# Performance work log

Hardware: AMD Instinct MI355X
Metric: run time of the kernel (lower is better)

Reference implementation:

```python
import jax, jax.numpy as jnp
import numpy as np

D_MODEL = 1024
NUM_HEADS = 16
D_HEAD = D_MODEL // NUM_HEADS


def setup_inputs() -> dict:
    key = jax.random.key(0)
    ks = jax.random.split(key, 5)
    b, n = 4, 2048
    x = jax.random.normal(ks[0], (b, n, D_MODEL), dtype=jnp.float32)
    s = 1.0 / np.sqrt(D_MODEL)
    w_qkv = jax.random.normal(ks[1], (D_MODEL, 3 * D_MODEL), dtype=jnp.float32) * s
    b_qkv = jax.random.normal(ks[2], (3 * D_MODEL,), dtype=jnp.float32) * 0.01
    w_out = jax.random.normal(ks[3], (D_MODEL, D_MODEL), dtype=jnp.float32) * s
    b_out = jax.random.normal(ks[4], (D_MODEL,), dtype=jnp.float32) * 0.01
    return {"x": x, "w_qkv": w_qkv, "b_qkv": b_qkv, "w_out": w_out, "b_out": b_out}


def reference(x, w_qkv, b_qkv, w_out, b_out):
    b, n, _ = x.shape
    h, d = NUM_HEADS, D_HEAD
    scale = d ** -0.5
    qkv = x @ w_qkv + b_qkv                       # [b, n, 3*d_model]
    # split as (qkv, h, d) on the feature axis, matching 'b n (qkv h d)'
    qkv = qkv.reshape(b, n, 3, h, d).transpose(2, 0, 3, 1, 4)  # [3, b, h, n, d]
    q, k, v = qkv[0], qkv[1], qkv[2]
    dots = jnp.einsum('bhid,bhjd->bhij', q, k) * scale
    causal = jnp.tril(jnp.ones((n, n), dtype=bool))
    dots = jnp.where(causal[None, None], dots, -jnp.inf)
    attn = jax.nn.softmax(dots, axis=-1)
    out = jnp.einsum('bhij,bhjd->bhid', attn, v)
    out = out.transpose(0, 2, 1, 3).reshape(b, n, h * d)
    return out @ w_out + b_out
```

## Files before the change

kernel.cpp:

```cpp
#include <hip/hip_runtime.h>
#include <hip/hip_bf16.h>
#include <stdint.h>

typedef unsigned short u16;
typedef __attribute__((ext_vector_type(8))) short bf16x8;
typedef __attribute__((ext_vector_type(4))) float f32x4;
typedef __attribute__((ext_vector_type(16))) float f32x16;
typedef __attribute__((ext_vector_type(4))) short s16x4;
typedef __attribute__((ext_vector_type(2))) unsigned u32x2;

#define SEQ   2048
#define BATCH 4

#define MFMA16(a,b,c) __builtin_amdgcn_mfma_f32_16x16x32_bf16(a,b,c,0,0,0)
#define MFMA32(a,b,c) __builtin_amdgcn_mfma_f32_32x32x16_bf16(a,b,c,0,0,0)
#define EXP2F __builtin_amdgcn_exp2f

__device__ __forceinline__ u16 f2bf(float f) {
  union { float f; uint32_t u; } c{f};
  uint32_t r = c.u + 0x7fffu + ((c.u >> 16) & 1u);
  return (u16)(r >> 16);
}

__device__ __forceinline__ void gll16(const void* g, void* l) {
  __builtin_amdgcn_global_load_lds((const __attribute__((address_space(1))) void*)g,
                                   (__attribute__((address_space(3))) void*)l,
                                   16, 0, 0);
}

__device__ __forceinline__ void plswap(uint32_t &a, uint32_t &b) {
  u32x2 r = __builtin_amdgcn_permlane32_swap(a, b, false, false);
  a = r[0]; b = r[1];
}
__device__ __forceinline__ float xhalf_max(float v) {
  union { float f; uint32_t u; } c{v};
  u32x2 r = __builtin_amdgcn_permlane32_swap(c.u, c.u, false, false);
  union { uint32_t u; float f; } x{r[0]}, y{r[1]};
  return fmaxf(x.f, y.f);
}
__device__ __forceinline__ float xhalf_add(float v) {
  union { float f; uint32_t u; } c{v};
  u32x2 r = __builtin_amdgcn_permlane32_swap(c.u, c.u, false, false);
  union { uint32_t u; float f; } x{r[0]}, y{r[1]};
  return x.f + y.f;
}

__global__ __launch_bounds__(256) void k_prep(const float* __restrict__ x,
                                              u16* __restrict__ xbf,
                                              const float* __restrict__ wqkv,
                                              u16* __restrict__ wqkvT,
                                              const float* __restrict__ wout,
                                              u16* __restrict__ woutT) {
  __shared__ float tl[32][33];
  const int bid = blockIdx.x, t = threadIdx.x;
  if (bid < 4096) {
    int i = (bid * 256 + t) * 8;
    float4 a = *(const float4*)(x + i);
    float4 b = *(const float4*)(x + i + 4);
    union { u16 u[8]; bf16x8 v; } r;
    r.u[0] = f2bf(a.x); r.u[1] = f2bf(a.y); r.u[2] = f2bf(a.z); r.u[3] = f2bf(a.w);
    r.u[4] = f2bf(b.x); r.u[5] = f2bf(b.y); r.u[6] = f2bf(b.z); r.u[7] = f2bf(b.w);
    *(bf16x8*)(xbf + i) = r.v;
    return;
  }
  const float* in; u16* out; int N, idx, nx;
  if (bid < 4096 + 3072) { in = wqkv; out = wqkvT; N = 3072; idx = bid - 4096; nx = 96; }
  else                   { in = wout; out = woutT; N = 1024; idx = bid - 7168; nx = 32; }
  const int K = 1024;
  const int c0 = (idx % nx) * 32, r0 = (idx / nx) * 32;
  const int tx = t & 31, ty = t >> 5;
#pragma unroll
  for (int j = 0; j < 32; j += 8)
    tl[ty + j][tx] = in[(size_t)(r0 + ty + j) * N + c0 + tx];
  __syncthreads();
#pragma unroll
  for (int j = 0; j < 32; j += 8)
    out[(size_t)(c0 + ty + j) * K + r0 + tx] = f2bf(tl[tx][ty + j]);
}

#define SBAR  asm volatile("s_barrier" ::: "memory")
#define LGKM0 asm volatile("s_waitcnt lgkmcnt(0)" ::: "memory")
#define VM2   asm volatile("s_waitcnt vmcnt(2)" ::: "memory")
#define VM0   asm volatile("s_waitcnt vmcnt(0)" ::: "memory")
#define FEN   asm volatile("" ::: "memory")

template<int OUT_F32, int VSPLIT>
__global__ __launch_bounds__(512, 2) void k_gemm256(const u16* __restrict__ A,
                                                    const u16* __restrict__ BT,
                                                    const float* __restrict__ bias,
                                                    void* __restrict__ Cv,
                                                    u16* __restrict__ vT,
                                                    int N, int K, int NT, int TN) {
  __shared__ alignas(16) char LDS[81920];
  const int t = threadIdx.x;
  const int l = t & 63, w = t >> 6;
  const int wm = w >> 2, wn = w & 3;
  const int lr = l & 15, lg = l >> 4;

  const int nwg = gridDim.x;
  const int cpx = nwg >> 3;
  const int sb = (blockIdx.x & 7) * cpx + (blockIdx.x >> 3);
  const int brow = (sb / TN) * 256, bcol = (sb % TN) * 128;

  auto stageA = [&](int c, int h, int tt) {
#pragma unroll
    for (int i = 0; i < 2; i++) {
      int s = t + i * 512;
      int r = s >> 3, cg = s & 7;
      int grow = brow + (r >> 6) * 128 + h * 64 + (r & 63);
      int gk = tt * 64 + ((cg ^ (r & 7)) * 8);
      gll16(A + (size_t)grow * K + gk, LDS + c * 32768 + h * 16384 + s * 16);
    }
  };
  auto stageB = [&](int tt) {
#pragma unroll
    for (int i = 0; i < 2; i++) {
      int s = t + i * 512;
      int r = s >> 3, cg = s & 7;
      int grow = bcol + r;
      int gk = tt * 64 + ((cg ^ (r & 7)) * 8);
      gll16(BT + (size_t)grow * K + gk, LDS + 65536 + s * 16);
    }
  };

  f32x4 acc[8][2] = {};
  bf16x8 afr[4], bfr[2][2];

#define READ_A(c, h, ks)                                                       \
  {                                                                            \
    const char* baseA = LDS + (c) * 32768 + (h) * 16384 + (wm * 64) * 128;     \
    _Pragma("unroll") for (int mi = 0; mi < 4; mi++)                           \
      afr[mi] = *(const bf16x8*)(baseA + (mi * 16 + lr) * 128 +                \
                                 ((((ks) * 4 + lg) ^ (lr & 7)) * 16));         \
  }
#define READ_B_ALL()                                                           \
  {                                                                            \
    const char* baseB = LDS + 65536 + (wn * 32) * 128;                         \
    _Pragma("unroll") for (int ks = 0; ks < 2; ks++)                           \
      _Pragma("unroll") for (int ni = 0; ni < 2; ni++)                         \
        bfr[ks][ni] = *(const bf16x8*)(baseB + (ni * 16 + lr) * 128 +          \
                                       (((ks * 4 + lg) ^ (lr & 7)) * 16));     \
  }
#define DO_MFMA(H, KS)                                                         \
  {                                                                            \
    __builtin_amdgcn_s_setprio(1);                                             \
    _Pragma("unroll") for (int mi = 0; mi < 4; mi++)                           \
      _Pragma("unroll") for (int ni = 0; ni < 2; ni++)                         \
        acc[(H)*4 + mi][ni] = MFMA16(afr[mi], bfr[KS][ni], acc[(H)*4 + mi][ni]); \
    __builtin_amdgcn_s_setprio(0);                                             \
  }

  stageA(0, 0, 0); FEN;
  stageB(0);       FEN;
  stageA(0, 1, 0); FEN;
  VM2; SBAR;

  for (int tt = 0; tt < NT; tt++) {
    const int c = tt & 1;
    if (tt + 1 < NT) { stageA(c ^ 1, 0, tt + 1); FEN; }
    READ_A(c, 0, 0); READ_B_ALL();
    DO_MFMA(0, 0);
    if (tt + 1 < NT) { VM2; } else { VM0; }
    LGKM0; SBAR;
    if (tt + 1 < NT) { stageB(tt + 1); FEN; }
    READ_A(c, 1, 0);
    DO_MFMA(1, 0);
    if (tt + 1 < NT) { stageA(c ^ 1, 1, tt + 1); FEN; }
    READ_A(c, 1, 1);
    DO_MFMA(1, 1);
    READ_A(c, 0, 1);
    DO_MFMA(0, 1);
    if (tt + 1 < NT) { VM2; } else { VM0; }
    LGKM0; SBAR;
  }

  const int r0 = brow + wm * 128 + lg * 4;
  const int c0 = bcol + wn * 32 + lr;
#pragma unroll
  for (int ni = 0; ni < 2; ni++) {
    const int col = c0 + ni * 16;
    float bv = bias[col];
#pragma unroll
    for (int mig = 0; mig < 8; mig++) {
      const int row = r0 + mig * 16;
      if (VSPLIT && col >= 2048) {
        const int bb = row >> 11, n0 = row & 2047;
        union { u16 u[4]; s16x4 v; } pk4;
#pragma unroll
        for (int r = 0; r < 4; r++) pk4.u[r] = f2bf(acc[mig][ni][r] + bv);
        *(s16x4*)(vT + ((size_t)(bb * 1024 + col - 2048) * SEQ + n0)) = pk4.v;
      } else {
#pragma unroll
        for (int r = 0; r < 4; r++) {
          float v = acc[mig][ni][r] + bv;
          size_t off = (size_t)(row + r) * N + col;
          if (OUT_F32) ((float*)Cv)[off] = v;
          else         ((u16*)Cv)[off]   = f2bf(v);
        }
      }
    }
  }
}
#undef READ_A
#undef READ_B_ALL
#undef DO_MFMA

__global__ __launch_bounds__(256, 2) void k_attn(const u16* __restrict__ qkv,
                                                 const u16* __restrict__ vT,
                                                 u16* __restrict__ outp) {
  __shared__ alignas(16) char SB[2][16384];
  const int t = threadIdx.x, l = t & 63, w = t >> 6;
  const int hi = l >> 5, q = l & 31;
  const int h = blockIdx.x, qp = blockIdx.y, b = blockIdx.z;
  const int bh = b * 16 + h;
  const int srow = t >> 3;
  const int csw = ((t & 7) * 16) ^ ((srow & 7) << 4);
  const int swz = (q & 7) << 4;
  const float SC = 0.18033688011112042f;

  auto STAGE = [&](char* buf, int kv0) {
    char* lK = buf + w * 1024;
    char* lV = buf + 8192 + w * 1024;
    gll16(qkv + (size_t)(b * SEQ + kv0 + srow) * 3072 + 1024 + h * 64 + (csw >> 1), lK);
    gll16(qkv + (size_t)(b * SEQ + kv0 + srow + 32) * 3072 + 1024 + h * 64 + (csw >> 1), lK + 4096);
    gll16(vT + (size_t)(bh * 64 + srow) * SEQ + kv0 + (csw >> 1), lV);
    gll16(vT + (size_t)(bh * 64 + srow + 32) * SEQ + kv0 + (csw >> 1), lV + 4096);
  };

  auto COMPUTE = [&](const char* Kb, const char* Vb, int kv0, int qr0, int qg,
                     const bf16x8* qf, f32x16& o0, f32x16& o1, f32x16& lv,
                     float& m_run) {
    f32x16 st0 = {}, st1 = {};
    __builtin_amdgcn_s_setprio(1);
#pragma unroll
    for (int c = 0; c < 4; c++) {
      const int cb = c * 32 + hi * 16;
      bf16x8 k0 = *(const bf16x8*)(Kb + q * 128 + (cb ^ swz));
      bf16x8 k1 = *(const bf16x8*)(Kb + (32 + q) * 128 + (cb ^ swz));
      st0 = MFMA32(k0, qf[c], st0);
      st1 = MFMA32(k1, qf[c], st1);
    }
    __builtin_amdgcn_s_setprio(0);
    if (kv0 + 63 > qr0) {
#pragma unroll
      for (int r = 0; r < 16; r++) {
        const int krow = (r & 3) + 8 * (r >> 2) + 4 * hi;
        if (kv0 + krow > qg)      st0[r] = -1e30f;
        if (kv0 + 32 + krow > qg) st1[r] = -1e30f;
      }
    }
    float tmx[16];
#pragma unroll
    for (int r = 0; r < 16; r++) tmx[r] = fmaxf(st0[r], st1[r]);
    float v0 = fmaxf(fmaxf(tmx[0], tmx[1]), tmx[2]);
    float v1 = fmaxf(fmaxf(tmx[3], tmx[4]), tmx[5]);
    float v2 = fmaxf(fmaxf(tmx[6], tmx[7]), tmx[8]);
    float v3 = fmaxf(fmaxf(tmx[9], tmx[10]), tmx[11]);
    float v4 = fmaxf(fmaxf(tmx[12], tmx[13]), tmx[14]);
    float v5 = fmaxf(fmaxf(v0, v1), tmx[15]);
    float v6 = fmaxf(fmaxf(v2, v3), v4);
    float v7 = fmaxf(v5, v6);
    const float vs = xhalf_max(v7) * SC;
    if (__any(vs > m_run + 8.0f)) {
      float mnew = fmaxf(m_run, vs);
      float corr = EXP2F(m_run - mnew);
      m_run = mnew;
#pragma unroll
      for (int r = 0; r < 16; r++) { o0[r] *= corr; o1[r] *= corr; lv[r] *= corr; }
    }
    f32x16 e0 = st0 * SC - m_run;
    f32x16 e1 = st1 * SC - m_run;
    f32x16 p0, p1;
#pragma unroll
    for (int r = 0; r < 16; r++) { p0[r] = EXP2F(e0[r]); p1[r] = EXP2F(e1[r]); }
    lv += p0 + p1;
#pragma unroll
    for (int khb = 0; khb < 2; khb++) {
      uint32_t pk[8];
#pragma unroll
      for (int ii = 0; ii < 8; ii++) {
        float lo = khb ? p1[2 * ii] : p0[2 * ii];
        float hf = khb ? p1[2 * ii + 1] : p0[2 * ii + 1];
        asm("v_cvt_pk_bf16_f32 %0, %1, %2" : "=v"(pk[ii]) : "v"(lo), "v"(hf));
      }
      plswap(pk[0], pk[2]); plswap(pk[1], pk[3]);
      plswap(pk[4], pk[6]); plswap(pk[5], pk[7]);
      union { uint32_t u[4]; bf16x8 v; } be, bo;
      be.u[0] = pk[0]; be.u[1] = pk[1]; be.u[2] = pk[2]; be.u[3] = pk[3];
      bo.u[0] = pk[4]; bo.u[1] = pk[5]; bo.u[2] = pk[6]; bo.u[3] = pk[7];
      __builtin_amdgcn_s_setprio(1);
#pragma unroll
      for (int kti = 0; kti < 2; kti++) {
        const int cb = (khb * 2 + kti) * 32 + hi * 16;
        bf16x8 vv0 = *(const bf16x8*)(Vb + q * 128 + (cb ^ swz));
        bf16x8 vv1 = *(const bf16x8*)(Vb + (32 + q) * 128 + (cb ^ swz));
        bf16x8 pb = kti ? bo.v : be.v;
        o0 = MFMA32(vv0, pb, o0);
        o1 = MFMA32(vv1, pb, o1);
      }
      __builtin_amdgcn_s_setprio(0);
    }
  };

  const int qtA = qp, qtB = 15 - qp;
  const int qr0A = qtA * 128 + w * 32, qgA = qr0A + q;
  const int qr0B = qtB * 128 + w * 32, qgB = qr0B + q;
  bf16x8 qfA[4], qfB[4];
#pragma unroll
  for (int c = 0; c < 4; c++) {
    qfA[c] = *(const bf16x8*)(qkv + (size_t)(b * SEQ + qgA) * 3072 + h * 64 + c * 16 + hi * 8);
    qfB[c] = *(const bf16x8*)(qkv + (size_t)(b * SEQ + qgB) * 3072 + h * 64 + c * 16 + hi * 8);
  }
  f32x16 oA0 = {}, oA1 = {}, lvA = {};
  f32x16 oB0 = {}, oB1 = {}, lvB = {};
  float mA = -1e30f, mB = -1e30f;
  const int nkvB = 2 * qtB + 2;

  STAGE(SB[0], 0);
  for (int j = 0; j < nkvB; j++) {
    const int kv0 = j * 64;
    __syncthreads();
    if (j + 1 < nkvB) STAGE(SB[(j + 1) & 1], kv0 + 64);
    const char* Kb = SB[j & 1];
    const char* Vb = Kb + 8192;
    if (kv0 <= qr0A + 31)
      COMPUTE(Kb, Vb, kv0, qr0A, qgA, qfA, oA0, oA1, lvA, mA);
    if (kv0 <= qr0B + 31)
      COMPUTE(Kb, Vb, kv0, qr0B, qgB, qfB, oB0, oB1, lvB, mB);
  }
#pragma unroll
  for (int sel = 0; sel < 2; sel++) {
    f32x16& o0 = sel ? oB0 : oA0;
    f32x16& o1 = sel ? oB1 : oA1;
    f32x16& lv = sel ? lvB : lvA;
    const int qg = sel ? qgB : qgA;
    float ls = ((lv[0] + lv[1]) + (lv[2] + lv[3])) + ((lv[4] + lv[5]) + (lv[6] + lv[7]))
             + ((lv[8] + lv[9]) + (lv[10] + lv[11])) + ((lv[12] + lv[13]) + (lv[14] + lv[15]));
    ls = xhalf_add(ls);
    const float invl = 1.0f / ls;
#pragma unroll
    for (int dh = 0; dh < 2; dh++)
#pragma unroll
      for (int jq = 0; jq < 4; jq++) {
        union { u16 u[4]; s16x4 v; } pk4;
#pragma unroll
        for (int r = 0; r < 4; r++)
          pk4.u[r] = f2bf((dh ? o1[4 * jq + r] : o0[4 * jq + r]) * invl);
        *(s16x4*)(outp + (size_t)(b * SEQ + qg) * 1024 + h * 64 + dh * 32 + jq * 8 + hi * 4) = pk4.v;
      }
  }
}

extern "C" void kernel_launch(void* const* d_in, const int* in_sizes, int n_in,
                              void* d_out, int out_size, void* d_ws, size_t ws_size,
                              hipStream_t stream) {
  const float* x     = (const float*)d_in[0];
  const float* w_qkv = (const float*)d_in[1];
  const float* b_qkv = (const float*)d_in[2];
  const float* w_out = (const float*)d_in[3];
  const float* b_out = (const float*)d_in[4];

  char* ws = (char*)d_ws;
  u16* xbf   = (u16*)(ws);
  u16* wqkvT = (u16*)(ws + (16u << 20));
  u16* woutT = (u16*)(ws + (22u << 20));
  u16* qkvb  = (u16*)(ws + (24u << 20));
  u16* vTb   = (u16*)(ws + (72u << 20));

  k_prep<<<8192, 256, 0, stream>>>(x, xbf, w_qkv, wqkvT, w_out, woutT);
  k_gemm256<0, 1><<<768, 512, 0, stream>>>(xbf, wqkvT, b_qkv, qkvb, vTb, 3072, 1024, 16, 24);
  k_attn<<<dim3(16, 8, 4), 256, 0, stream>>>(qkvb, vTb, xbf);
  k_gemm256<1, 0><<<256, 512, 0, stream>>>(xbf, woutT, b_out, d_out, nullptr, 1024, 1024, 16, 8);
}
```

Measured before the change: 157.6 us.

## Single-buffer second A half-tile in GEMM to cut LDS footprint

Shrinks the GEMM shared-memory allocation from 80KB to 64KB by keeping only the first 64-row half of the A tile double-buffered. The second half is now loaded into a single buffer at the start of each k-iteration, and the loop drains all outstanding loads at the end of every iteration. The aim is to lower LDS pressure and perhaps ease residency or allocation. In exchange, the load latency of the second A half is exposed within each iteration instead of being prefetched one iteration ahead.

```diff
diff --git a/kernel.cpp b/kernel.cpp
--- a/kernel.cpp
+++ b/kernel.cpp
@@ -91,7 +91,7 @@
                                                     void* __restrict__ Cv,
                                                     u16* __restrict__ vT,
                                                     int N, int K, int NT, int TN) {
-  __shared__ alignas(16) char LDS[81920];
+  __shared__ alignas(16) char LDS[65536];
   const int t = threadIdx.x;
   const int l = t & 63, w = t >> 6;
   const int wm = w >> 2, wn = w & 3;
@@ -102,14 +102,24 @@
   const int sb = (blockIdx.x & 7) * cpx + (blockIdx.x >> 3);
   const int brow = (sb / TN) * 256, bcol = (sb % TN) * 128;
 
-  auto stageA = [&](int c, int h, int tt) {
+  auto stageA0 = [&](int c, int tt) {
 #pragma unroll
     for (int i = 0; i < 2; i++) {
       int s = t + i * 512;
       int r = s >> 3, cg = s & 7;
-      int grow = brow + (r >> 6) * 128 + h * 64 + (r & 63);
+      int grow = brow + (r >> 6) * 128 + (r & 63);
       int gk = tt * 64 + ((cg ^ (r & 7)) * 8);
-      gll16(A + (size_t)grow * K + gk, LDS + c * 32768 + h * 16384 + s * 16);
+      gll16(A + (size_t)grow * K + gk, LDS + c * 16384 + s * 16);
+    }
+  };
+  auto stageA1 = [&](int tt) {
+#pragma unroll
+    for (int i = 0; i < 2; i++) {
+      int s = t + i * 512;
+      int r = s >> 3, cg = s & 7;
+      int grow = brow + (r >> 6) * 128 + 64 + (r & 63);
+      int gk = tt * 64 + ((cg ^ (r & 7)) * 8);
+      gll16(A + (size_t)grow * K + gk, LDS + 32768 + s * 16);
     }
   };
   auto stageB = [&](int tt) {
@@ -119,23 +129,30 @@
       int r = s >> 3, cg = s & 7;
       int grow = bcol + r;
       int gk = tt * 64 + ((cg ^ (r & 7)) * 8);
-      gll16(BT + (size_t)grow * K + gk, LDS + 65536 + s * 16);
+      gll16(BT + (size_t)grow * K + gk, LDS + 49152 + s * 16);
     }
   };
 
   f32x4 acc[8][2] = {};
   bf16x8 afr[4], bfr[2][2];
 
-#define READ_A(c, h, ks)                                                       \
+#define READ_A0(c, ks)                                                         \
   {                                                                            \
-    const char* baseA = LDS + (c) * 32768 + (h) * 16384 + (wm * 64) * 128;     \
+    const char* baseA = LDS + (c) * 16384 + (wm * 64) * 128;                   \
     _Pragma("unroll") for (int mi = 0; mi < 4; mi++)                           \
       afr[mi] = *(const bf16x8*)(baseA + (mi * 16 + lr) * 128 +                \
                                  ((((ks) * 4 + lg) ^ (lr & 7)) * 16));         \
   }
+#define READ_A1(ks)                                                            \
+  {                                                                            \
+    const char* baseA = LDS + 32768 + (wm * 64) * 128;                         \
+    _Pragma("unroll") for (int mi = 0; mi < 4; mi++)                           \
+      afr[mi] = *(const bf16x8*)(baseA + (mi * 16 + lr) * 128 +                \
+                                 ((((ks) * 4 + lg) ^ (lr & 7)) * 16));         \
+  }
 #define READ_B_ALL()                                                           \
   {                                                                            \
-    const char* baseB = LDS + 65536 + (wn * 32) * 128;                         \
+    const char* baseB = LDS + 49152 + (wn * 32) * 128;                         \
     _Pragma("unroll") for (int ks = 0; ks < 2; ks++)                           \
       _Pragma("unroll") for (int ni = 0; ni < 2; ni++)                         \
         bfr[ks][ni] = *(const bf16x8*)(baseB + (ni * 16 + lr) * 128 +          \
@@ -150,27 +167,26 @@
     __builtin_amdgcn_s_setprio(0);                                             \
   }
 
-  stageA(0, 0, 0); FEN;
-  stageB(0);       FEN;
-  stageA(0, 1, 0); FEN;
-  VM2; SBAR;
+  stageA0(0, 0); FEN;
+  stageB(0);     FEN;
+  VM0; SBAR;
 
   for (int tt = 0; tt < NT; tt++) {
     const int c = tt & 1;
-    if (tt + 1 < NT) { stageA(c ^ 1, 0, tt + 1); FEN; }
-    READ_A(c, 0, 0); READ_B_ALL();
+    stageA1(tt); FEN;
+    if (tt + 1 < NT) { stageA0(c ^ 1, tt + 1); FEN; }
+    READ_A0(c, 0); READ_B_ALL();
     DO_MFMA(0, 0);
     if (tt + 1 < NT) { VM2; } else { VM0; }
     LGKM0; SBAR;
     if (tt + 1 < NT) { stageB(tt + 1); FEN; }
-    READ_A(c, 1, 0);
+    READ_A1(0);
     DO_MFMA(1, 0);
-    if (tt + 1 < NT) { stageA(c ^ 1, 1, tt + 1); FEN; }
-    READ_A(c, 1, 1);
+    READ_A1(1);
     DO_MFMA(1, 1);
-    READ_A(c, 0, 1);
+    READ_A0(c, 1);
     DO_MFMA(0, 1);
-    if (tt + 1 < NT) { VM2; } else { VM0; }
+    VM0;
     LGKM0; SBAR;
   }
 
@@ -201,7 +217,8 @@
     }
   }
 }
-#undef READ_A
+#undef READ_A0
+#undef READ_A1
 #undef READ_B_ALL
 #undef DO_MFMA
 
```

After: 162.5 us. +3.1%, slower.
